# Kernel tuning notes

Measured on AMD Instinct MI355X. Metric: run time of the kernel, lower is better.

## Reference

```python
import jax, jax.numpy as jnp
import numpy as np

B, IN, K, E = 2048, 1024, 128, 64  # batch, in_features, n_concepts, emb_size


def setup_inputs() -> dict:
    key = jax.random.key(0)
    k1, k2, k3, k4, k5 = jax.random.split(key, 5)
    x = jax.random.normal(k1, (B, IN), dtype=jnp.float32)
    # stacked per-concept Linear(in_features, 2*emb_size)
    W = jax.random.normal(k2, (K, IN, 2 * E), dtype=jnp.float32) * (1.0 / np.sqrt(IN))
    b = jax.random.normal(k3, (K, 2 * E), dtype=jnp.float32) * 0.01
    # shared prob predictor Linear(2*emb_size, 1)
    wp = jax.random.normal(k4, (2 * E,), dtype=jnp.float32) * (1.0 / np.sqrt(2 * E))
    bp = jax.random.normal(k5, (), dtype=jnp.float32) * 0.01
    return {"x": x, "W": W, "b": b, "wp": wp, "bp": bp}


def reference(x, W, b, wp, bp):
    # batched GEMM over all concepts at once: [B,K,2E]
    context = jax.nn.leaky_relu(jnp.einsum('bi,kio->bko', x, W) + b)
    # shared predictor + sigmoid: [B,K]
    c_pred = jax.nn.sigmoid(jnp.einsum('bko,o->bk', context, wp) + bp)
    ctx_pos = context[..., :E]
    ctx_neg = context[..., E:]
    p = c_pred[..., None]
    c_emb = ctx_pos * p + ctx_neg * (1.0 - p)  # [B,K,E]
    return c_emb, c_pred
```

## Files before the change

kernel.cpp:

```cpp
#include <hip/hip_runtime.h>

typedef unsigned int u32;
typedef unsigned short u16;
typedef __attribute__((ext_vector_type(8))) __bf16 bf16x8;
typedef __attribute__((ext_vector_type(4))) float f32x4;

#define B_SZ 2048
#define IN_SZ 1024
#define K_SZ 128
#define E_SZ 64
#define TWOE 128
static const size_t OUT_EMB = (size_t)B_SZ * K_SZ * E_SZ;

__device__ __forceinline__ u16 f2bf(float f) {
    u32 u = __builtin_bit_cast(u32, f);
    u32 r = u + 0x7fffu + ((u >> 16) & 1u);
    return (u16)(r >> 16);
}

__device__ __forceinline__ void async16(const void* g, void* l) {
    __builtin_amdgcn_global_load_lds((const __attribute__((address_space(1))) u32*)g,
                                     (__attribute__((address_space(3))) u32*)l, 16, 0, 0);
}

__global__ void __launch_bounds__(256) cvt_x(const float* __restrict__ in, u16* __restrict__ outp, int n4) {
    int i = blockIdx.x * blockDim.x + threadIdx.x;
    if (i < n4) {
        float4 v = ((const float4*)in)[i];
        u32 lo = (u32)f2bf(v.x) | ((u32)f2bf(v.y) << 16);
        u32 hi = (u32)f2bf(v.z) | ((u32)f2bf(v.w) << 16);
        ((uint2*)outp)[i] = make_uint2(lo, hi);
    }
}

__global__ void __launch_bounds__(256) cvt_w(const float* __restrict__ W, u16* __restrict__ wt) {
    __shared__ u16 tr[128][72];
    const int k = blockIdx.y, i0 = blockIdx.x * 64;
    const float* src = W + (size_t)k * IN_SZ * TWOE + (size_t)i0 * TWOE;
#pragma unroll
    for (int r = 0; r < 8; ++r) {
        int idx = r * 256 + threadIdx.x;
        int i = idx >> 5;
        int o = (idx & 31) * 4;
        float4 v = ((const float4*)src)[idx];
        tr[o + 0][i] = f2bf(v.x);
        tr[o + 1][i] = f2bf(v.y);
        tr[o + 2][i] = f2bf(v.z);
        tr[o + 3][i] = f2bf(v.w);
    }
    __syncthreads();
    const int o = threadIdx.x >> 1, h = threadIdx.x & 1;
    u16* dst = wt + ((size_t)(k * TWOE + o) * IN_SZ) + i0 + h * 32;
#pragma unroll
    for (int s = 0; s < 4; ++s) {
        uint4 v = *(const uint4*)&tr[o][h * 32 + s * 8];
        ((uint4*)dst)[s] = v;
    }
}

__global__ void __launch_bounds__(256) cvt_pred(const float* __restrict__ pw, float* __restrict__ out) {
    __shared__ float t[128][132];
    const int b0 = blockIdx.x * 128;
    const int tid = threadIdx.x;
#pragma unroll
    for (int i = 0; i < 16; ++i) {
        int idx = i * 256 + tid;
        int kk = idx >> 5, c4 = (idx & 31) * 4;
        float4 v = *(const float4*)(pw + (size_t)kk * B_SZ + b0 + c4);
        t[kk][c4 + 0] = v.x; t[kk][c4 + 1] = v.y; t[kk][c4 + 2] = v.z; t[kk][c4 + 3] = v.w;
    }
    __syncthreads();
#pragma unroll
    for (int i = 0; i < 16; ++i) {
        int idx = i * 256 + tid;
        int bl = idx >> 5, k4 = (idx & 31) * 4;
        float4 v = make_float4(t[k4 + 0][bl], t[k4 + 1][bl], t[k4 + 2][bl], t[k4 + 3][bl]);
        *(float4*)(out + OUT_EMB + (size_t)(b0 + bl) * K_SZ + k4) = v;
    }
}

__global__ void __launch_bounds__(512, 2) fused_main(
    const u16* __restrict__ xb,
    const u16* __restrict__ wt,
    const float* __restrict__ bias, const float* __restrict__ wpv,
    const float* __restrict__ bpp, float* __restrict__ out,
    float* __restrict__ pw) {
    __shared__ union {
        u16 stage[65536];
        struct { float pl[2][256][2]; float ex[2][256][66]; } epi;
    } sm;
    char* smb = (char*)&sm;

    const int tid = threadIdx.x;
    const int l = tid & 63, w = tid >> 6;
    const int wm = w >> 2, wn = w & 3;
    const int hi = l >> 4, lo16 = l & 15;
    const int q = l >> 2;
    const int swz = (l & 3) ^ ((l >> 3) & 3);

    const int id = blockIdx.x;
    const int xcd = id & 7, j = id >> 3;
    const int kp = (xcd << 3) | (j >> 3);
    const int brow = (j & 7) << 8;

    const u16* abase = xb + (size_t)(brow + w * 16 + q) * IN_SZ + swz * 8;
    const u16* bbase = wt + ((size_t)kp * 256 + w * 16 + q) * IN_SZ + swz * 8;

    const int xsl = (hi ^ ((lo16 >> 1) & 3)) << 4;

    f32x4 acc[8][4] = {};

    auto SA = [&](int d, int kh, int t) {
        u16* dst = (u16*)&sm + (d * 2 + kh) * 8192 + w * 512;
        const u16* src = abase + t * 64 + kh * 32;
        async16(src, dst);
        async16(src + (size_t)128 * IN_SZ, dst + 4096);
    };
    auto SB = [&](int d, int kh, int t) {
        u16* dst = (u16*)&sm + 32768 + (d * 2 + kh) * 8192 + w * 512;
        const u16* src = bbase + t * 64 + kh * 32;
        async16(src, dst);
        async16(src + (size_t)128 * IN_SZ, dst + 4096);
    };

    auto PHN = [&](int d, int kh) {
        const char* ra = smb + (d * 2 + kh) * 16384;
        const char* rb = smb + 65536 + (d * 2 + kh) * 16384;
        bf16x8 af[8], bfr[4];
#pragma unroll
        for (int n = 0; n < 4; ++n)
            bfr[n] = *(const bf16x8*)(rb + (wn * 64 + n * 16 + lo16) * 64 + xsl);
#pragma unroll
        for (int mm = 0; mm < 8; ++mm)
            af[mm] = *(const bf16x8*)(ra + (wm * 128 + mm * 16 + lo16) * 64 + xsl);
        __builtin_amdgcn_s_setprio(1);
#pragma unroll
        for (int mm = 0; mm < 8; ++mm)
#pragma unroll
            for (int n = 0; n < 4; ++n)
                acc[mm][n] = __builtin_amdgcn_mfma_f32_16x16x32_bf16(
                    af[mm], bfr[n], acc[mm][n], 0, 0, 0);
        __builtin_amdgcn_s_setprio(0);
    };

    const int khf = wm;

    SA(0, 0, 0); SB(0, 0, 0); SA(0, 1, 0); SB(0, 1, 0);
    asm volatile("s_waitcnt vmcnt(0)" ::: "memory");
    __builtin_amdgcn_s_barrier();

#pragma unroll 1
    for (int t = 0; t < 16; ++t) {
        const int d = t & 1, dn = d ^ 1;
        if (t < 15) {
            SA(dn, 0, t + 1); SB(dn, 0, t + 1);
            SA(dn, 1, t + 1); SB(dn, 1, t + 1);
            asm volatile("" ::: "memory");
        }
        PHN(d, khf);
        PHN(d, khf ^ 1);
        asm volatile("s_waitcnt vmcnt(0)" ::: "memory");
        __builtin_amdgcn_s_barrier();
    }

    const int ksel = wn >> 1, oh = wn & 1;
    const int kglob = kp * 2 + ksel;
    const float bp_val = *bpp;
    float bvals[4], wvals[4];
#pragma unroll
    for (int n = 0; n < 4; ++n) {
        const int o = oh * 64 + n * 16 + lo16;
        bvals[n] = bias[kglob * TWOE + o];
        wvals[n] = wpv[o];
    }
    float p[8][4];
#pragma unroll
    for (int m = 0; m < 8; ++m)
#pragma unroll
        for (int jj = 0; jj < 4; ++jj) {
            float s = 0.f;
#pragma unroll
            for (int n = 0; n < 4; ++n) {
                float v = acc[m][n][jj] + bvals[n];
                v = v > 0.f ? v : 0.01f * v;
                acc[m][n][jj] = v;
                s += v * wvals[n];
            }
            s += __shfl_xor(s, 1);
            s += __shfl_xor(s, 2);
            s += __shfl_xor(s, 4);
            s += __shfl_xor(s, 8);
            p[m][jj] = s;
        }
    if (lo16 == 0) {
#pragma unroll
        for (int m = 0; m < 8; ++m)
#pragma unroll
            for (int jj = 0; jj < 4; ++jj)
                sm.epi.pl[ksel][wm * 128 + m * 16 + hi * 4 + jj][oh] = p[m][jj];
    }
    __builtin_amdgcn_s_barrier();
#pragma unroll
    for (int m = 0; m < 8; ++m)
#pragma unroll
        for (int jj = 0; jj < 4; ++jj) {
            const int rg = wm * 128 + m * 16 + hi * 4 + jj;
            const float z = sm.epi.pl[ksel][rg][0] + sm.epi.pl[ksel][rg][1] + bp_val;
            p[m][jj] = 1.f / (1.f + __expf(-z));
        }
    if (oh == 0 && lo16 == 0) {
        if (pw) {
#pragma unroll
            for (int m = 0; m < 8; ++m) {
                float4 v = make_float4(p[m][0], p[m][1], p[m][2], p[m][3]);
                *(float4*)(pw + (size_t)kglob * B_SZ + brow + wm * 128 + m * 16 + hi * 4) = v;
            }
        } else {
#pragma unroll
            for (int m = 0; m < 8; ++m)
#pragma unroll
                for (int jj = 0; jj < 4; ++jj) {
                    const int b = brow + wm * 128 + m * 16 + hi * 4 + jj;
                    out[OUT_EMB + (size_t)b * K_SZ + kglob] = p[m][jj];
                }
        }
    }
    if (oh == 1) {
#pragma unroll
        for (int m = 0; m < 8; ++m)
#pragma unroll
            for (int n = 0; n < 4; ++n)
#pragma unroll
                for (int jj = 0; jj < 4; ++jj)
                    sm.epi.ex[ksel][wm * 128 + m * 16 + hi * 4 + jj][n * 16 + lo16] =
                        (1.f - p[m][jj]) * acc[m][n][jj];
    }
    __builtin_amdgcn_s_barrier();
    if (oh == 0) {
#pragma unroll
        for (int m = 0; m < 8; ++m)
#pragma unroll
            for (int n = 0; n < 4; ++n)
#pragma unroll
                for (int jj = 0; jj < 4; ++jj) {
                    const int rl = wm * 128 + m * 16 + hi * 4 + jj;
                    const int b = brow + rl;
                    const int e = n * 16 + lo16;
                    out[((size_t)b * K_SZ + kglob) * E_SZ + e] =
                        p[m][jj] * acc[m][n][jj] + sm.epi.ex[ksel][rl][e];
                }
    }
}

__global__ void __launch_bounds__(128) fallback_kernel(
    const float* __restrict__ x, const float* __restrict__ W,
    const float* __restrict__ bias, const float* __restrict__ wpv,
    const float* __restrict__ bpp, float* __restrict__ out) {
    const int k = blockIdx.y;
    const int b0 = blockIdx.x * 8;
    const int o = threadIdx.x;
    __shared__ float xs[8][1024];
    __shared__ float red[2];
    __shared__ float exch[64];
    for (int idx = threadIdx.x; idx < 8 * 1024; idx += 128)
        xs[idx >> 10][idx & 1023] = x[(size_t)(b0 + (idx >> 10)) * IN_SZ + (idx & 1023)];
    __syncthreads();
    float a[8] = {};
    for (int i = 0; i < 1024; ++i) {
        float wv = W[((size_t)k * IN_SZ + i) * TWOE + o];
#pragma unroll
        for (int bb = 0; bb < 8; ++bb) a[bb] += xs[bb][i] * wv;
    }
    const float bo = bias[k * TWOE + o], wo = wpv[o], bpv = *bpp;
    for (int bb = 0; bb < 8; ++bb) {
        float c = a[bb] + bo;
        c = c > 0.f ? c : 0.01f * c;
        float s = c * wo;
        for (int off = 1; off < 64; off <<= 1) s += __shfl_xor(s, off);
        if ((threadIdx.x & 63) == 0) red[threadIdx.x >> 6] = s;
        __syncthreads();
        float p = 1.f / (1.f + expf(-(red[0] + red[1] + bpv)));
        if (o >= 64) exch[o - 64] = (1.f - p) * c;
        __syncthreads();
        if (o < 64) out[((size_t)(b0 + bb) * K_SZ + k) * E_SZ + o] = p * c + exch[o];
        if (o == 0) out[OUT_EMB + (size_t)(b0 + bb) * K_SZ + k] = p;
        __syncthreads();
    }
}

extern "C" void kernel_launch(void* const* d_in, const int* in_sizes, int n_in,
                              void* d_out, int out_size, void* d_ws, size_t ws_size,
                              hipStream_t stream) {
    const float* x = (const float*)d_in[0];
    const float* W = (const float*)d_in[1];
    const float* bias = (const float*)d_in[2];
    const float* wp = (const float*)d_in[3];
    const float* bp = (const float*)d_in[4];
    float* out = (float*)d_out;

    const size_t X_ELEMS = (size_t)B_SZ * IN_SZ;
    const size_t WT_ELEMS = (size_t)K_SZ * TWOE * IN_SZ;
    const size_t PW_ELEMS = (size_t)K_SZ * B_SZ;
    const size_t NEED_BASE = (X_ELEMS + WT_ELEMS) * sizeof(u16);
    const size_t NEED_FULL = NEED_BASE + PW_ELEMS * sizeof(float);

    if (ws_size >= NEED_BASE) {
        u16* xb = (u16*)d_ws;
        u16* wt = xb + X_ELEMS;
        float* pw = (ws_size >= NEED_FULL) ? (float*)(wt + WT_ELEMS) : nullptr;
        int n4 = (int)(X_ELEMS / 4);
        cvt_x<<<dim3((n4 + 255) / 256), 256, 0, stream>>>(x, xb, n4);
        cvt_w<<<dim3(16, 128), 256, 0, stream>>>(W, wt);
        fused_main<<<dim3(512), 512, 0, stream>>>(xb, wt, bias, wp, bp, out, pw);
        if (pw) cvt_pred<<<dim3(16), 256, 0, stream>>>(pw, out);
    } else {
        fallback_kernel<<<dim3(B_SZ / 8, K_SZ), 128, 0, stream>>>(x, W, bias, wp, bp, out);
    }
}
```

Before: 115.7 us.

## Swap GEMM operands so each wave owns a full concept's outputs in registers

Swaps the A and B operands of the MFMA tile, so W rows map to the M dimension and batch rows to N. Each wave (indexed by wm) then holds all 128 output features of one concept for its batch columns. The predictor dot product and the positive/negative mix can be done in registers with two cross-lane shuffles. This removes the LDS exchange buffers, the extra barriers and the scalar scattered stores. The embedding output becomes float4 stores, and bias and wp are read as float4. Risk: the pw and c_pred stores now come from lanes 0-15 only, and the register layout changes.

```diff
diff --git a/kernel.cpp b/kernel.cpp
--- a/kernel.cpp
+++ b/kernel.cpp
@@ -85,11 +85,8 @@
     const float* __restrict__ bias, const float* __restrict__ wpv,
     const float* __restrict__ bpp, float* __restrict__ out,
     float* __restrict__ pw) {
-    __shared__ union {
-        u16 stage[65536];
-        struct { float pl[2][256][2]; float ex[2][256][66]; } epi;
-    } sm;
-    char* smb = (char*)&sm;
+    __shared__ u16 smst[65536];
+    char* smb = (char*)&smst[0];
 
     const int tid = threadIdx.x;
     const int l = tid & 63, w = tid >> 6;
@@ -103,21 +100,21 @@
     const int kp = (xcd << 3) | (j >> 3);
     const int brow = (j & 7) << 8;
 
-    const u16* abase = xb + (size_t)(brow + w * 16 + q) * IN_SZ + swz * 8;
-    const u16* bbase = wt + ((size_t)kp * 256 + w * 16 + q) * IN_SZ + swz * 8;
+    const u16* abase = wt + ((size_t)kp * 256 + w * 16 + q) * IN_SZ + swz * 8;
+    const u16* bbase = xb + (size_t)(brow + w * 16 + q) * IN_SZ + swz * 8;
 
     const int xsl = (hi ^ ((lo16 >> 1) & 3)) << 4;
 
     f32x4 acc[8][4] = {};
 
     auto SA = [&](int d, int kh, int t) {
-        u16* dst = (u16*)&sm + (d * 2 + kh) * 8192 + w * 512;
+        u16* dst = &smst[0] + (d * 2 + kh) * 8192 + w * 512;
         const u16* src = abase + t * 64 + kh * 32;
         async16(src, dst);
         async16(src + (size_t)128 * IN_SZ, dst + 4096);
     };
     auto SB = [&](int d, int kh, int t) {
-        u16* dst = (u16*)&sm + 32768 + (d * 2 + kh) * 8192 + w * 512;
+        u16* dst = &smst[0] + 32768 + (d * 2 + kh) * 8192 + w * 512;
         const u16* src = bbase + t * 64 + kh * 32;
         async16(src, dst);
         async16(src + (size_t)128 * IN_SZ, dst + 4096);
@@ -142,8 +139,6 @@
                     af[mm], bfr[n], acc[mm][n], 0, 0, 0);
         __builtin_amdgcn_s_setprio(0);
     };
-
-    const int khf = wm;
 
     SA(0, 0, 0); SB(0, 0, 0); SA(0, 1, 0); SB(0, 1, 0);
     asm volatile("s_waitcnt vmcnt(0)" ::: "memory");
@@ -157,98 +152,65 @@
             SA(dn, 1, t + 1); SB(dn, 1, t + 1);
             asm volatile("" ::: "memory");
         }
-        PHN(d, khf);
-        PHN(d, khf ^ 1);
+        PHN(d, 0);
+        PHN(d, 1);
         asm volatile("s_waitcnt vmcnt(0)" ::: "memory");
         __builtin_amdgcn_s_barrier();
     }
 
-    const int ksel = wn >> 1, oh = wn & 1;
-    const int kglob = kp * 2 + ksel;
+    const int kglob = kp * 2 + wm;
     const float bp_val = *bpp;
-    float bvals[4], wvals[4];
+    float4 b4[8], w4[8];
+#pragma unroll
+    for (int m = 0; m < 8; ++m) {
+        b4[m] = *(const float4*)(bias + kglob * TWOE + m * 16 + hi * 4);
+        w4[m] = *(const float4*)(wpv + m * 16 + hi * 4);
+    }
+    float pn[4];
 #pragma unroll
     for (int n = 0; n < 4; ++n) {
-        const int o = oh * 64 + n * 16 + lo16;
-        bvals[n] = bias[kglob * TWOE + o];
-        wvals[n] = wpv[o];
-    }
-    float p[8][4];
-#pragma unroll
-    for (int m = 0; m < 8; ++m)
-#pragma unroll
-        for (int jj = 0; jj < 4; ++jj) {
-            float s = 0.f;
-#pragma unroll
-            for (int n = 0; n < 4; ++n) {
-                float v = acc[m][n][jj] + bvals[n];
-                v = v > 0.f ? v : 0.01f * v;
-                acc[m][n][jj] = v;
-                s += v * wvals[n];
-            }
-            s += __shfl_xor(s, 1);
-            s += __shfl_xor(s, 2);
-            s += __shfl_xor(s, 4);
-            s += __shfl_xor(s, 8);
-            p[m][jj] = s;
-        }
-    if (lo16 == 0) {
-#pragma unroll
-        for (int m = 0; m < 8; ++m)
-#pragma unroll
-            for (int jj = 0; jj < 4; ++jj)
-                sm.epi.pl[ksel][wm * 128 + m * 16 + hi * 4 + jj][oh] = p[m][jj];
-    }
-    __builtin_amdgcn_s_barrier();
-#pragma unroll
-    for (int m = 0; m < 8; ++m)
-#pragma unroll
-        for (int jj = 0; jj < 4; ++jj) {
-            const int rg = wm * 128 + m * 16 + hi * 4 + jj;
-            const float z = sm.epi.pl[ksel][rg][0] + sm.epi.pl[ksel][rg][1] + bp_val;
-            p[m][jj] = 1.f / (1.f + __expf(-z));
-        }
-    if (oh == 0 && lo16 == 0) {
+        float s = 0.f;
+#pragma unroll
+        for (int m = 0; m < 8; ++m) {
+            f32x4 v = acc[m][n];
+            float t0 = v[0] + b4[m].x; t0 = t0 > 0.f ? t0 : 0.01f * t0;
+            float t1 = v[1] + b4[m].y; t1 = t1 > 0.f ? t1 : 0.01f * t1;
+            float t2 = v[2] + b4[m].z; t2 = t2 > 0.f ? t2 : 0.01f * t2;
+            float t3 = v[3] + b4[m].w; t3 = t3 > 0.f ? t3 : 0.01f * t3;
+            v[0] = t0; v[1] = t1; v[2] = t2; v[3] = t3;
+            acc[m][n] = v;
+            s += t0 * w4[m].x + t1 * w4[m].y + t2 * w4[m].z + t3 * w4[m].w;
+        }
+        s += __shfl_xor(s, 16);
+        s += __shfl_xor(s, 32);
+        pn[n] = 1.f / (1.f + __expf(-(s + bp_val)));
+    }
+    if (hi == 0) {
         if (pw) {
 #pragma unroll
-            for (int m = 0; m < 8; ++m) {
-                float4 v = make_float4(p[m][0], p[m][1], p[m][2], p[m][3]);
-                *(float4*)(pw + (size_t)kglob * B_SZ + brow + wm * 128 + m * 16 + hi * 4) = v;
-            }
+            for (int n = 0; n < 4; ++n)
+                pw[(size_t)kglob * B_SZ + brow + wn * 64 + n * 16 + lo16] = pn[n];
         } else {
 #pragma unroll
-            for (int m = 0; m < 8; ++m)
-#pragma unroll
-                for (int jj = 0; jj < 4; ++jj) {
-                    const int b = brow + wm * 128 + m * 16 + hi * 4 + jj;
-                    out[OUT_EMB + (size_t)b * K_SZ + kglob] = p[m][jj];
-                }
-        }
-    }
-    if (oh == 1) {
-#pragma unroll
-        for (int m = 0; m < 8; ++m)
-#pragma unroll
             for (int n = 0; n < 4; ++n)
-#pragma unroll
-                for (int jj = 0; jj < 4; ++jj)
-                    sm.epi.ex[ksel][wm * 128 + m * 16 + hi * 4 + jj][n * 16 + lo16] =
-                        (1.f - p[m][jj]) * acc[m][n][jj];
-    }
-    __builtin_amdgcn_s_barrier();
-    if (oh == 0) {
-#pragma unroll
-        for (int m = 0; m < 8; ++m)
-#pragma unroll
-            for (int n = 0; n < 4; ++n)
-#pragma unroll
-                for (int jj = 0; jj < 4; ++jj) {
-                    const int rl = wm * 128 + m * 16 + hi * 4 + jj;
-                    const int b = brow + rl;
-                    const int e = n * 16 + lo16;
-                    out[((size_t)b * K_SZ + kglob) * E_SZ + e] =
-                        p[m][jj] * acc[m][n][jj] + sm.epi.ex[ksel][rl][e];
-                }
+                out[OUT_EMB + (size_t)(brow + wn * 64 + n * 16 + lo16) * K_SZ + kglob] = pn[n];
+        }
+    }
+#pragma unroll
+    for (int n = 0; n < 4; ++n) {
+        const size_t bb = (size_t)(brow + wn * 64 + n * 16 + lo16);
+        float* op = out + (bb * K_SZ + kglob) * E_SZ + hi * 4;
+        const float pv = pn[n], qv = 1.f - pn[n];
+#pragma unroll
+        for (int mp = 0; mp < 4; ++mp) {
+            f32x4 cp = acc[mp][n], cn = acc[mp + 4][n];
+            f32x4 r;
+            r[0] = pv * cp[0] + qv * cn[0];
+            r[1] = pv * cp[1] + qv * cn[1];
+            r[2] = pv * cp[2] + qv * cn[2];
+            r[3] = pv * cp[3] + qv * cn[3];
+            *(f32x4*)(op + mp * 16) = r;
+        }
     }
 }
 
```

Measured after the change: 109.7 us. 5.2% less time.
